# Kernel optimization log

Measured on AMD Instinct MI355X. Metric: run time of the kernel, lower is better.

Reference implementation:

```python
import jax, jax.numpy as jnp
import numpy as np

D_K = 64  # from init_kwargs

def setup_inputs() -> dict:
    key = jax.random.key(0)
    k1, k2, k3 = jax.random.split(key, 3)
    B, H, S = 2, 16, 2048
    q = jax.random.normal(k1, (B, H, S, D_K), dtype=jnp.float32)
    k = jax.random.normal(k2, (B, H, D_K, S), dtype=jnp.float32)
    v = jax.random.normal(k3, (B, H, S, D_K), dtype=jnp.float32)
    return {"q": q, "k": k, "v": v}

def reference(q, k, v):
    # scores = q @ k / sqrt(d_k)  -> [B,H,S,S]; k is pre-transposed [B,H,d_k,S]
    scale = 1.0 / (D_K ** 0.5)
    scores = jnp.einsum('bhsd,bhdt->bhst', q, k) * scale
    attn = jax.nn.softmax(scores, axis=-1)
    context = jnp.einsum('bhst,bhtd->bhsd', attn, v)
    return (context, attn)
```

## Files before the change

kernel.cpp:

```cpp
#include <hip/hip_runtime.h>

typedef __attribute__((ext_vector_type(4))) float    f32x4;
typedef __attribute__((ext_vector_type(8))) short    short8;
typedef __attribute__((ext_vector_type(4))) unsigned uint4v;

#define BH_   32
#define S_    2048
#define DK_   64
#define TQ_   128
#define NT_   256
#define C_    64
#define NCH_  (S_ / C_)
#define NBLK_ (BH_ * (S_ / TQ_))
#define SCALE_LOG2E 0.18033688011112042f

#define QP_ELEMS (BH_ * 128 * 64 * 16)
#define KP_ELEMS (BH_ * NCH_ * 8 * 64 * 8)
#define VP_ELEMS KP_ELEMS
#define WS_NEEDED ((size_t)(QP_ELEMS + KP_ELEMS + VP_ELEMS) * 2)

#define PROW_  68
#define PPLANE_ (16 * PROW_)

__device__ __forceinline__ unsigned short f2bf(float x) {
    unsigned u = __builtin_bit_cast(unsigned, x);
    u += 0x7FFFu + ((u >> 16) & 1u);
    return (unsigned short)(u >> 16);
}
__device__ __forceinline__ float e2(float x) { return __builtin_amdgcn_exp2f(x); }

__global__ __launch_bounds__(256)
void sdpa_prepack_kernel(const float* __restrict__ q, const float* __restrict__ k,
                         const float* __restrict__ v, unsigned short* __restrict__ qp,
                         unsigned short* __restrict__ kp, unsigned short* __restrict__ vp)
{
    const int bid = blockIdx.x;
    const int tid = threadIdx.x;
    if (bid < 2048) {
        const int i  = bid * 256 + tid;
        const int sl = i & 63, s = (i >> 6) & 7, ch = (i >> 9) & 31, bh = i >> 14;
        const int sg = sl >> 4, sn = sl & 15;
        const float* base = k + (size_t)bh * DK_ * S_
                              + (size_t)(32 * (s & 1) + 8 * sg) * S_
                              + ch * C_ + 16 * (s >> 1) + sn;
        short8 t;
#pragma unroll
        for (int j = 0; j < 8; ++j) t[j] = (short)f2bf(base[(size_t)j * S_]);
        *(short8*)&kp[(size_t)i * 8] = t;
    } else if (bid < 4096) {
        const int i  = (bid - 2048) * 256 + tid;
        const int sl = i & 63, s = (i >> 6) & 7, ch = (i >> 9) & 31, bh = i >> 14;
        const int sg = sl >> 4, sn = sl & 15;
        const float* base = v + (size_t)bh * S_ * DK_
                              + (size_t)(ch * C_ + 32 * (s & 1) + 4 * sg) * DK_
                              + 16 * (s >> 1) + sn;
        short8 t;
#pragma unroll
        for (int j = 0; j < 4; ++j) {
            t[j]     = (short)f2bf(base[(size_t)j * DK_]);
            t[4 + j] = (short)f2bf(base[(size_t)(16 + j) * DK_]);
        }
        *(short8*)&vp[(size_t)i * 8] = t;
    } else {
        const int i  = (bid - 4096) * 256 + tid;
        const int l  = i & 63, tg = (i >> 6) & 127, bh = i >> 13;
        const int g  = l >> 4, ln = l & 15;
        const float* qr = q + ((size_t)bh * S_ + tg * 16 + ln) * DK_;
        short8 t0, t1;
#pragma unroll
        for (int j = 0; j < 8; ++j) {
            t0[j] = (short)f2bf(qr[8 * g + j]      * SCALE_LOG2E);
            t1[j] = (short)f2bf(qr[32 + 8 * g + j] * SCALE_LOG2E);
        }
        *(short8*)&qp[(size_t)i * 16]     = t0;
        *(short8*)&qp[(size_t)i * 16 + 8] = t1;
    }
}

__global__ __launch_bounds__(NT_)
void sdpa_main_kernel(const unsigned short* __restrict__ qp,
                      const unsigned short* __restrict__ kp,
                      const unsigned short* __restrict__ vp,
                      float* __restrict__ ctx, float* __restrict__ attn)
{
    __shared__ float plds[4 * PPLANE_];

    const int tid = threadIdx.x;
    const int w   = tid >> 6;
    const int l   = tid & 63;
    const int g   = l >> 4;
    const int ln  = l & 15;

    float* pl = &plds[w * PPLANE_];

    const int orig = blockIdx.x;
    const int bid  = (orig & 7) * 64 + (orig >> 3);

    const int bh   = bid >> 4;
    const int qb   = bid & 15;
    const int row0 = qb * TQ_;

    const unsigned short* kph = kp + (size_t)bh * (NCH_ * 8 * 64 * 8) + (size_t)l * 8;
    const unsigned short* vph = vp + (size_t)bh * (NCH_ * 8 * 64 * 8) + (size_t)l * 8;

    short8 aq[2][2];
#pragma unroll
    for (int rt = 0; rt < 2; ++rt) {
        const size_t qi = ((size_t)(bh * 128 + qb * 8 + w * 2 + rt) * 64 + l) * 16;
        aq[rt][0] = *(const short8*)&qp[qi];
        aq[rt][1] = *(const short8*)&qp[qi + 8];
    }

    short8 kfA[8], kfB[8];

    float lsum0 = 0.f;
#pragma unroll
    for (int s = 0; s < 8; ++s)
        kfA[s] = *(const short8*)(kph + (size_t)s * 512);

#define SUM0(KF)                                                                \
    _Pragma("unroll")                                                           \
    for (int ct = 0; ct < 4; ++ct) {                                            \
        f32x4 acc = {0.f, 0.f, 0.f, 0.f};                                       \
        acc = __builtin_amdgcn_mfma_f32_16x16x32_bf16(KF[2*ct],   aq[0][0], acc, 0, 0, 0); \
        acc = __builtin_amdgcn_mfma_f32_16x16x32_bf16(KF[2*ct+1], aq[0][1], acc, 0, 0, 0); \
        lsum0 += (e2(acc[0]) + e2(acc[1])) + (e2(acc[2]) + e2(acc[3]));         \
    }

    for (int ch = 0; ch < NCH_; ch += 2) {
#pragma unroll
        for (int s = 0; s < 8; ++s)
            kfB[s] = *(const short8*)(kph + ((size_t)(ch + 1) * 8 + s) * 512);
        SUM0(kfA)
        if (ch + 2 < NCH_) {
#pragma unroll
            for (int s = 0; s < 8; ++s)
                kfA[s] = *(const short8*)(kph + ((size_t)(ch + 2) * 8 + s) * 512);
        }
        SUM0(kfB)
    }
#undef SUM0
    lsum0 += __shfl_xor(lsum0, 16);
    lsum0 += __shfl_xor(lsum0, 32);
    const float lrec0 = 1.0f / lsum0;

    f32x4 cacc[2][4];
#pragma unroll
    for (int rt = 0; rt < 2; ++rt)
#pragma unroll
        for (int dt = 0; dt < 4; ++dt) cacc[rt][dt] = (f32x4){0.f, 0.f, 0.f, 0.f};

    float lsum1 = 0.f;
    float* attwb0 = attn + ((size_t)bh * S_ + row0 + w * 32 + (l >> 4)) * S_ + (l & 15) * 4;
    float* attwb1 = attwb0 + (size_t)16 * S_;

#pragma unroll
    for (int s = 0; s < 8; ++s)
        kfA[s] = *(const short8*)(kph + (size_t)s * 512);

#define PHB(CH, KF, VF)                                                         \
    {                                                                           \
        const int c0 = (CH) * C_;                                               \
        unsigned pau0[2][4], pau1[2][4];                                        \
        _Pragma("unroll")                                                       \
        for (int ct = 0; ct < 4; ++ct) {                                        \
            const int kb2 = ct >> 1, hf = ct & 1;                               \
            f32x4 a0 = {0.f, 0.f, 0.f, 0.f};                                    \
            a0 = __builtin_amdgcn_mfma_f32_16x16x32_bf16(KF[2*ct],   aq[0][0], a0, 0, 0, 0); \
            a0 = __builtin_amdgcn_mfma_f32_16x16x32_bf16(KF[2*ct+1], aq[0][1], a0, 0, 0, 0); \
            f32x4 p;                                                            \
            _Pragma("unroll")                                                   \
            for (int r = 0; r < 4; ++r) p[r] = e2(a0[r]) * lrec0;               \
            *(f32x4*)&pl[ln * PROW_ + 16 * ct + 4 * g] = p;                     \
            pau0[kb2][hf * 2 + 0] = (unsigned)f2bf(p[0]) | ((unsigned)f2bf(p[1]) << 16); \
            pau0[kb2][hf * 2 + 1] = (unsigned)f2bf(p[2]) | ((unsigned)f2bf(p[3]) << 16); \
            f32x4 a1 = {0.f, 0.f, 0.f, 0.f};                                    \
            a1 = __builtin_amdgcn_mfma_f32_16x16x32_bf16(KF[2*ct],   aq[1][0], a1, 0, 0, 0); \
            a1 = __builtin_amdgcn_mfma_f32_16x16x32_bf16(KF[2*ct+1], aq[1][1], a1, 0, 0, 0); \
            f32x4 e;                                                            \
            _Pragma("unroll")                                                   \
            for (int r = 0; r < 4; ++r) e[r] = e2(a1[r]);                       \
            lsum1 += (e[0] + e[1]) + (e[2] + e[3]);                             \
            pau1[kb2][hf * 2 + 0] = (unsigned)f2bf(e[0]) | ((unsigned)f2bf(e[1]) << 16); \
            pau1[kb2][hf * 2 + 1] = (unsigned)f2bf(e[2]) | ((unsigned)f2bf(e[3]) << 16); \
        }                                                                       \
        _Pragma("unroll")                                                       \
        for (int kb2 = 0; kb2 < 2; ++kb2) {                                     \
            uint4v pw0 = {pau0[kb2][0], pau0[kb2][1], pau0[kb2][2], pau0[kb2][3]}; \
            uint4v pw1 = {pau1[kb2][0], pau1[kb2][1], pau1[kb2][2], pau1[kb2][3]}; \
            const short8 pa0 = __builtin_bit_cast(short8, pw0);                 \
            const short8 pa1 = __builtin_bit_cast(short8, pw1);                 \
            _Pragma("unroll")                                                   \
            for (int dt = 0; dt < 4; ++dt) {                                    \
                cacc[0][dt] = __builtin_amdgcn_mfma_f32_16x16x32_bf16(pa0, VF[dt * 2 + kb2], cacc[0][dt], 0, 0, 0); \
                cacc[1][dt] = __builtin_amdgcn_mfma_f32_16x16x32_bf16(pa1, VF[dt * 2 + kb2], cacc[1][dt], 0, 0, 0); \
            }                                                                   \
        }                                                                       \
                   \
        _Pragma("unroll")                                                       \
        for (int u = 0; u < 4; ++u) {                                           \
            const f32x4 pr = *(const f32x4*)&pl[(4 * u + (l >> 4)) * PROW_ + 4 * (l & 15)]; \
            __builtin_nontemporal_store(pr,                                     \
                (f32x4*)(attwb0 + (size_t)(4 * u) * S_ + c0));                  \
        }                                                                       \
    }

    for (int ch = 0; ch < NCH_; ch += 2) {
        short8 vfA[8];
#pragma unroll
        for (int s = 0; s < 8; ++s)
            vfA[s] = *(const short8*)(vph + ((size_t)ch * 8 + s) * 512);
#pragma unroll
        for (int s = 0; s < 8; ++s)
            kfB[s] = *(const short8*)(kph + ((size_t)(ch + 1) * 8 + s) * 512);
        PHB(ch, kfA, vfA)

        short8 vfB[8];
#pragma unroll
        for (int s = 0; s < 8; ++s)
            vfB[s] = *(const short8*)(vph + ((size_t)(ch + 1) * 8 + s) * 512);
        if (ch + 2 < NCH_) {
#pragma unroll
            for (int s = 0; s < 8; ++s)
                kfA[s] = *(const short8*)(kph + ((size_t)(ch + 2) * 8 + s) * 512);
        }
        PHB(ch + 1, kfB, vfB)
    }
#undef PHB

    lsum1 += __shfl_xor(lsum1, 16);
    lsum1 += __shfl_xor(lsum1, 32);
    const float lrec1 = 1.0f / lsum1;

#pragma unroll
    for (int s = 0; s < 8; ++s)
        kfA[s] = *(const short8*)(kph + (size_t)s * 512);

#define PHC(CH, KF)                                                             \
    {                                                                           \
        const int c0 = (CH) * C_;                                               \
        _Pragma("unroll")                                                       \
        for (int ct = 0; ct < 4; ++ct) {                                        \
            f32x4 a1 = {0.f, 0.f, 0.f, 0.f};                                    \
            a1 = __builtin_amdgcn_mfma_f32_16x16x32_bf16(KF[2*ct],   aq[1][0], a1, 0, 0, 0); \
            a1 = __builtin_amdgcn_mfma_f32_16x16x32_bf16(KF[2*ct+1], aq[1][1], a1, 0, 0, 0); \
            f32x4 p;                                                            \
            _Pragma("unroll")                                                   \
            for (int r = 0; r < 4; ++r) p[r] = e2(a1[r]) * lrec1;               \
            *(f32x4*)&pl[ln * PROW_ + 16 * ct + 4 * g] = p;                     \
        }                                                                       \
        _Pragma("unroll")                                                       \
        for (int u = 0; u < 4; ++u) {                                           \
            const f32x4 pr = *(const f32x4*)&pl[(4 * u + (l >> 4)) * PROW_ + 4 * (l & 15)]; \
            __builtin_nontemporal_store(pr,                                     \
                (f32x4*)(attwb1 + (size_t)(4 * u) * S_ + c0));                  \
        }                                                                       \
    }

    for (int ch = 0; ch < NCH_; ch += 2) {
#pragma unroll
        for (int s = 0; s < 8; ++s)
            kfB[s] = *(const short8*)(kph + ((size_t)(ch + 1) * 8 + s) * 512);
        PHC(ch, kfA)
        if (ch + 2 < NCH_) {
#pragma unroll
            for (int s = 0; s < 8; ++s)
                kfA[s] = *(const short8*)(kph + ((size_t)(ch + 2) * 8 + s) * 512);
        }
        PHC(ch + 1, kfB)
    }
#undef PHC

#pragma unroll
    for (int rt = 0; rt < 2; ++rt) {
        float* cw = ctx + ((size_t)bh * S_ + row0 + w * 32 + rt * 16 + 4 * g) * DK_ + ln;
#pragma unroll
        for (int r = 0; r < 4; ++r) {
            const float sc = (rt == 0) ? 1.0f : __shfl(lrec1, 4 * g + r);
#pragma unroll
            for (int dt = 0; dt < 4; ++dt)
                __builtin_nontemporal_store(cacc[rt][dt][r] * sc,
                                            cw + (size_t)r * DK_ + 16 * dt);
        }
    }
}

__global__ __launch_bounds__(NT_, 4)
void sdpa_fallback_kernel(const float* __restrict__ q, const float* __restrict__ k,
                          const float* __restrict__ v, float* __restrict__ ctx,
                          float* __restrict__ attn)
{
    __shared__ unsigned short klds[8 * 64 * 8];
    __shared__ unsigned short vlds[8 * 64 * 8];

    const int tid = threadIdx.x;
    const int w   = tid >> 6;
    const int l   = tid & 63;
    const int g   = l >> 4;
    const int ln  = l & 15;

    const int bh   = blockIdx.x >> 5;
    const int qb   = blockIdx.x & 31;
    const int row0 = qb * 64;

    const float* kb = k + (size_t)bh * DK_ * S_;
    const float* vb = v + (size_t)bh * S_ * DK_;

    const int s0 = tid >> 6;
    const int sl = tid & 63;
    const int sg = sl >> 4, sn = sl & 15;

    const float* kg0 = kb + (size_t)(32 * (s0 & 1) + 8 * sg) * S_ + 16 * (s0 >> 1) + sn;
    const float* kg1 = kb + (size_t)(32 * (s0 & 1) + 8 * sg) * S_ + 16 * ((s0 + 4) >> 1) + sn;
    const float* vg0 = vb + (size_t)(32 * (s0 & 1) + 4 * sg) * DK_ + 16 * (s0 >> 1) + sn;
    const float* vg1 = vb + (size_t)(32 * (s0 & 1) + 4 * sg) * DK_ + 16 * ((s0 + 4) >> 1) + sn;

    unsigned short* kw0 = &klds[((s0    ) * 64 + sl) * 8];
    unsigned short* kw1 = &klds[((s0 + 4) * 64 + sl) * 8];
    unsigned short* vw0 = &vlds[((s0    ) * 64 + sl) * 8];
    unsigned short* vw1 = &vlds[((s0 + 4) * 64 + sl) * 8];

    auto stageK = [&](const float* base, unsigned short* dst, int c0) {
        short8 t;
#pragma unroll
        for (int j = 0; j < 8; ++j)
            t[j] = (short)f2bf(base[(size_t)j * S_ + c0]);
        *(short8*)dst = t;
    };
    auto stageV = [&](const float* base, unsigned short* dst, int t0) {
        short8 t;
#pragma unroll
        for (int j = 0; j < 4; ++j) {
            t[j]     = (short)f2bf(base[(size_t)(t0 + j) * DK_]);
            t[4 + j] = (short)f2bf(base[(size_t)(t0 + 16 + j) * DK_]);
        }
        *(short8*)dst = t;
    };

    const float* qrow = q + ((size_t)bh * S_ + row0 + w * 16 + ln) * DK_;
    short8 aq0, aq1;
#pragma unroll
    for (int j = 0; j < 8; ++j) {
        aq0[j] = (short)f2bf(qrow[g * 8 + j]      * SCALE_LOG2E);
        aq1[j] = (short)f2bf(qrow[g * 8 + 32 + j] * SCALE_LOG2E);
    }

    float lsum = 0.f;
    for (int ch = 0; ch < NCH_; ++ch) {
        const int c0 = ch * C_;
        __syncthreads();
        stageK(kg0, kw0, c0);
        stageK(kg1, kw1, c0);
        __syncthreads();
#pragma unroll
        for (int ct = 0; ct < 4; ++ct) {
            const short8 kf0 = *(const short8*)&klds[((ct * 2 + 0) * 64 + l) * 8];
            const short8 kf1 = *(const short8*)&klds[((ct * 2 + 1) * 64 + l) * 8];
            f32x4 acc = {0.f, 0.f, 0.f, 0.f};
            acc = __builtin_amdgcn_mfma_f32_16x16x32_bf16(kf0, aq0, acc, 0, 0, 0);
            acc = __builtin_amdgcn_mfma_f32_16x16x32_bf16(kf1, aq1, acc, 0, 0, 0);
            lsum += (e2(acc[0]) + e2(acc[1])) + (e2(acc[2]) + e2(acc[3]));
        }
    }
    lsum += __shfl_xor(lsum, 16);
    lsum += __shfl_xor(lsum, 32);
    const float lrec = 1.0f / lsum;

    f32x4 cacc[4];
#pragma unroll
    for (int dt = 0; dt < 4; ++dt) cacc[dt] = (f32x4){0.f, 0.f, 0.f, 0.f};

    float* attw = attn + ((size_t)bh * S_ + row0 + w * 16 + ln) * S_ + 4 * g;

    for (int ch = 0; ch < NCH_; ++ch) {
        const int c0 = ch * C_;
        __syncthreads();
        stageK(kg0, kw0, c0);
        stageK(kg1, kw1, c0);
        stageV(vg0, vw0, c0);
        stageV(vg1, vw1, c0);
        __syncthreads();

        unsigned pau[2][4];
#pragma unroll
        for (int ct = 0; ct < 4; ++ct) {
            const short8 kf0 = *(const short8*)&klds[((ct * 2 + 0) * 64 + l) * 8];
            const short8 kf1 = *(const short8*)&klds[((ct * 2 + 1) * 64 + l) * 8];
            f32x4 acc = {0.f, 0.f, 0.f, 0.f};
            acc = __builtin_amdgcn_mfma_f32_16x16x32_bf16(kf0, aq0, acc, 0, 0, 0);
            acc = __builtin_amdgcn_mfma_f32_16x16x32_bf16(kf1, aq1, acc, 0, 0, 0);

            f32x4 p;
#pragma unroll
            for (int r = 0; r < 4; ++r) p[r] = e2(acc[r]) * lrec;
            *(f32x4*)(attw + c0 + 16 * ct) = p;

            const int kb2 = ct >> 1, hf = ct & 1;
            pau[kb2][hf * 2 + 0] = (unsigned)f2bf(p[0]) | ((unsigned)f2bf(p[1]) << 16);
            pau[kb2][hf * 2 + 1] = (unsigned)f2bf(p[2]) | ((unsigned)f2bf(p[3]) << 16);
        }

#pragma unroll
        for (int kb2 = 0; kb2 < 2; ++kb2) {
            uint4v pw = {pau[kb2][0], pau[kb2][1], pau[kb2][2], pau[kb2][3]};
            const short8 pa = __builtin_bit_cast(short8, pw);
#pragma unroll
            for (int dt = 0; dt < 4; ++dt) {
                const short8 vf = *(const short8*)&vlds[((dt * 2 + kb2) * 64 + l) * 8];
                cacc[dt] = __builtin_amdgcn_mfma_f32_16x16x32_bf16(pa, vf, cacc[dt], 0, 0, 0);
            }
        }
    }

    float* cw = ctx + ((size_t)bh * S_ + row0 + w * 16 + 4 * g) * DK_ + ln;
#pragma unroll
    for (int dt = 0; dt < 4; ++dt)
#pragma unroll
        for (int r = 0; r < 4; ++r)
            cw[(size_t)r * DK_ + 16 * dt] = cacc[dt][r];
}

extern "C" void kernel_launch(void* const* d_in, const int* in_sizes, int n_in,
                              void* d_out, int out_size, void* d_ws, size_t ws_size,
                              hipStream_t stream)
{
    const float* q = (const float*)d_in[0];
    const float* k = (const float*)d_in[1];
    const float* v = (const float*)d_in[2];
    float* ctx  = (float*)d_out;
    float* attn = (float*)d_out + (size_t)BH_ * S_ * DK_;

    if (ws_size >= WS_NEEDED) {
        unsigned short* qp = (unsigned short*)d_ws;
        unsigned short* kp = qp + QP_ELEMS;
        unsigned short* vp = kp + KP_ELEMS;
        sdpa_prepack_kernel<<<dim3(5120), dim3(256), 0, stream>>>(q, k, v, qp, kp, vp);
        sdpa_main_kernel<<<dim3(NBLK_), dim3(NT_), 0, stream>>>(qp, kp, vp, ctx, attn);
    } else {
        sdpa_fallback_kernel<<<dim3(BH_ * 32), dim3(NT_), 0, stream>>>(q, k, v, ctx, attn);
    }
}
```

Measured before the change: 152.2 us.

## Double-buffer LDS attention tiles and defer writeback by one chunk

Doubles the per-wave LDS plane so each chunk's probabilities go to one buffer while the previous chunk's tile is read back and streamed to global memory. The writeback therefore sits one chunk behind the compute, separating the LDS write from the dependent LDS read. It also raises wave priority around the MFMA sections with s_setprio. In exchange, LDS use per block doubles, which could lower occupancy, and the final chunk needs an extra tail writeback.

```diff
diff --git a/kernel.cpp b/kernel.cpp
--- a/kernel.cpp
+++ b/kernel.cpp
@@ -83,7 +83,7 @@
                       const unsigned short* __restrict__ vp,
                       float* __restrict__ ctx, float* __restrict__ attn)
 {
-    __shared__ float plds[4 * PPLANE_];
+    __shared__ float plds[4 * 2 * PPLANE_];
 
     const int tid = threadIdx.x;
     const int w   = tid >> 6;
@@ -91,7 +91,8 @@
     const int g   = l >> 4;
     const int ln  = l & 15;
 
-    float* pl = &plds[w * PPLANE_];
+    float* pl0 = &plds[w * 2 * PPLANE_];
+    float* pl1 = pl0 + PPLANE_;
 
     const int orig = blockIdx.x;
     const int bid  = (orig & 7) * 64 + (orig >> 3);
@@ -158,10 +159,18 @@
     for (int s = 0; s < 8; ++s)
         kfA[s] = *(const short8*)(kph + (size_t)s * 512);
 
-#define PHB(CH, KF, VF)                                                         \
+#define WB(PLR, C0P, ATTB)                                                      \
+    _Pragma("unroll")                                                           \
+    for (int u = 0; u < 4; ++u) {                                               \
+        const f32x4 pr = *(const f32x4*)&(PLR)[(4 * u + (l >> 4)) * PROW_ + 4 * (l & 15)]; \
+        __builtin_nontemporal_store(pr, (f32x4*)((ATTB) + (size_t)(4 * u) * S_ + (C0P))); \
+    }
+
+#define PHB(CH, KF, VF, PLW, PLR, DOWB)                                         \
     {                                                                           \
-        const int c0 = (CH) * C_;                                               \
+        if (DOWB) { WB(PLR, ((CH) - 1) * C_, attwb0) }                          \
         unsigned pau0[2][4], pau1[2][4];                                        \
+        __builtin_amdgcn_s_setprio(1);                                          \
         _Pragma("unroll")                                                       \
         for (int ct = 0; ct < 4; ++ct) {                                        \
             const int kb2 = ct >> 1, hf = ct & 1;                               \
@@ -171,7 +180,7 @@
             f32x4 p;                                                            \
             _Pragma("unroll")                                                   \
             for (int r = 0; r < 4; ++r) p[r] = e2(a0[r]) * lrec0;               \
-            *(f32x4*)&pl[ln * PROW_ + 16 * ct + 4 * g] = p;                     \
+            *(f32x4*)&(PLW)[ln * PROW_ + 16 * ct + 4 * g] = p;                  \
             pau0[kb2][hf * 2 + 0] = (unsigned)f2bf(p[0]) | ((unsigned)f2bf(p[1]) << 16); \
             pau0[kb2][hf * 2 + 1] = (unsigned)f2bf(p[2]) | ((unsigned)f2bf(p[3]) << 16); \
             f32x4 a1 = {0.f, 0.f, 0.f, 0.f};                                    \
@@ -196,13 +205,7 @@
                 cacc[1][dt] = __builtin_amdgcn_mfma_f32_16x16x32_bf16(pa1, VF[dt * 2 + kb2], cacc[1][dt], 0, 0, 0); \
             }                                                                   \
         }                                                                       \
-                   \
-        _Pragma("unroll")                                                       \
-        for (int u = 0; u < 4; ++u) {                                           \
-            const f32x4 pr = *(const f32x4*)&pl[(4 * u + (l >> 4)) * PROW_ + 4 * (l & 15)]; \
-            __builtin_nontemporal_store(pr,                                     \
-                (f32x4*)(attwb0 + (size_t)(4 * u) * S_ + c0));                  \
-        }                                                                       \
+        __builtin_amdgcn_s_setprio(0);                                          \
     }
 
     for (int ch = 0; ch < NCH_; ch += 2) {
@@ -213,7 +216,7 @@
 #pragma unroll
         for (int s = 0; s < 8; ++s)
             kfB[s] = *(const short8*)(kph + ((size_t)(ch + 1) * 8 + s) * 512);
-        PHB(ch, kfA, vfA)
+        PHB(ch, kfA, vfA, pl0, pl1, ch > 0)
 
         short8 vfB[8];
 #pragma unroll
@@ -224,9 +227,10 @@
             for (int s = 0; s < 8; ++s)
                 kfA[s] = *(const short8*)(kph + ((size_t)(ch + 2) * 8 + s) * 512);
         }
-        PHB(ch + 1, kfB, vfB)
+        PHB(ch + 1, kfB, vfB, pl1, pl0, true)
     }
 #undef PHB
+    WB(pl1, (NCH_ - 1) * C_, attwb0)
 
     lsum1 += __shfl_xor(lsum1, 16);
     lsum1 += __shfl_xor(lsum1, 32);
@@ -236,9 +240,10 @@
     for (int s = 0; s < 8; ++s)
         kfA[s] = *(const short8*)(kph + (size_t)s * 512);
 
-#define PHC(CH, KF)                                                             \
+#define PHC(CH, KF, PLW, PLR, DOWB)                                             \
     {                                                                           \
-        const int c0 = (CH) * C_;                                               \
+        if (DOWB) { WB(PLR, ((CH) - 1) * C_, attwb1) }                          \
+        __builtin_amdgcn_s_setprio(1);                                          \
         _Pragma("unroll")                                                       \
         for (int ct = 0; ct < 4; ++ct) {                                        \
             f32x4 a1 = {0.f, 0.f, 0.f, 0.f};                                    \
@@ -247,29 +252,26 @@
             f32x4 p;                                                            \
             _Pragma("unroll")                                                   \
             for (int r = 0; r < 4; ++r) p[r] = e2(a1[r]) * lrec1;               \
-            *(f32x4*)&pl[ln * PROW_ + 16 * ct + 4 * g] = p;                     \
+            *(f32x4*)&(PLW)[ln * PROW_ + 16 * ct + 4 * g] = p;                  \
         }                                                                       \
-        _Pragma("unroll")                                                       \
-        for (int u = 0; u < 4; ++u) {                                           \
-            const f32x4 pr = *(const f32x4*)&pl[(4 * u + (l >> 4)) * PROW_ + 4 * (l & 15)]; \
-            __builtin_nontemporal_store(pr,                                     \
-                (f32x4*)(attwb1 + (size_t)(4 * u) * S_ + c0));                  \
-        }                                                                       \
+        __builtin_amdgcn_s_setprio(0);                                          \
     }
 
     for (int ch = 0; ch < NCH_; ch += 2) {
 #pragma unroll
         for (int s = 0; s < 8; ++s)
             kfB[s] = *(const short8*)(kph + ((size_t)(ch + 1) * 8 + s) * 512);
-        PHC(ch, kfA)
+        PHC(ch, kfA, pl0, pl1, ch > 0)
         if (ch + 2 < NCH_) {
 #pragma unroll
             for (int s = 0; s < 8; ++s)
                 kfA[s] = *(const short8*)(kph + ((size_t)(ch + 2) * 8 + s) * 512);
         }
-        PHC(ch + 1, kfB)
+        PHC(ch + 1, kfB, pl1, pl0, true)
     }
 #undef PHC
+    WB(pl1, (NCH_ - 1) * C_, attwb1)
+#undef WB
 
 #pragma unroll
     for (int rt = 0; rt < 2; ++rt) {
```

Result: no change. 150.4 us (-1.2%).
